# Performance work log

Hardware: AMD Instinct MI355X
Metric: run time of the kernel (lower is better)

The kernel has to match this reference:

```python
import jax, jax.numpy as jnp
import numpy as np

EPS = 1e-5

def layer_norm(x, g, b):
    m = x.mean(-1, keepdims=True)
    v = ((x - m) ** 2).mean(-1, keepdims=True)
    return (x - m) / jnp.sqrt(v + EPS) * g + b

def multihead(qn, kn, vn, Wq, Wk, Wv, causal):
    # Wq/Wk/Wv: [H, E, D]; per-head projections stacked over H (matches per-head Linear loop)
    Q = jnp.einsum('ble,hed->bhld', qn, Wq)
    K = jnp.einsum('bme,hed->bhmd', kn, Wk)
    V = jnp.einsum('bme,hed->bhmd', vn, Wv)
    scale = Q.shape[-1] ** -0.5
    s = jnp.einsum('bhld,bhmd->bhlm', Q, K) * scale
    if causal:
        L, M = s.shape[-2], s.shape[-1]
        mask = jnp.tril(jnp.ones((L, M), dtype=bool))
        s = jnp.where(mask, s, -jnp.inf)
    w = jax.nn.softmax(s, axis=-1)
    o = jnp.einsum('bhlm,bhmd->bhld', w, V)
    return o.mean(axis=1)  # heads are AVERAGED, not concatenated


def setup_inputs() -> dict:
    key = jax.random.key(0)
    ks = jax.random.split(key, 16)
    B, L, E, H, D, FW = 4, 2048, 512, 8, 512, 4
    std = 0.02
    inp = {
        'q': jax.random.normal(ks[0], (B, L, E), jnp.float32),
        'k': jax.random.normal(ks[1], (B, L, E), jnp.float32),
        'v': jax.random.normal(ks[2], (B, L, E), jnp.float32),
        'Wq_s': jax.random.normal(ks[3], (H, E, D), jnp.float32) * std,
        'Wk_s': jax.random.normal(ks[4], (H, E, D), jnp.float32) * std,
        'Wv_s': jax.random.normal(ks[5], (H, E, D), jnp.float32) * std,
        'Wq_c': jax.random.normal(ks[6], (H, E, D), jnp.float32) * std,
        'Wk_c': jax.random.normal(ks[7], (H, E, D), jnp.float32) * std,
        'Wv_c': jax.random.normal(ks[8], (H, E, D), jnp.float32) * std,
        'W1': jax.random.normal(ks[9], (E, FW * E), jnp.float32) * std,
        'b1': jnp.zeros((FW * E,), jnp.float32),
        'W2': jax.random.normal(ks[10], (FW * E, E), jnp.float32) * std,
        'b2': jnp.zeros((E,), jnp.float32),
        'g1': jnp.ones((E,), jnp.float32), 'be1': jnp.zeros((E,), jnp.float32),
        'g2': jnp.ones((E,), jnp.float32), 'be2': jnp.zeros((E,), jnp.float32),
        'g3': jnp.ones((E,), jnp.float32), 'be3': jnp.zeros((E,), jnp.float32),
    }
    return inp


def reference(q, k, v, Wq_s, Wk_s, Wv_s, Wq_c, Wk_c, Wv_c, W1, b1, W2, b2,
              g1, be1, g2, be2, g3, be3):
    # pre-norm causal self-attn (head_size == n_embd, heads averaged)
    q = q + multihead(layer_norm(q, g1, be1), layer_norm(q, g1, be1), layer_norm(q, g1, be1),
                      Wq_s, Wk_s, Wv_s, causal=True)
    # pre-norm cross-attn: only queries are normed; k, v used raw
    q = q + multihead(layer_norm(q, g2, be2), k, v, Wq_c, Wk_c, Wv_c, causal=False)
    # FFN
    h = layer_norm(q, g3, be3)
    h = jax.nn.relu(h @ W1 + b1) @ W2 + b2
    return q + h
```

## Files before the change

kernel.cpp:

```cpp
#include <hip/hip_runtime.h>
#include <cstdint>


typedef __bf16 bf16;
typedef __bf16 bf16x8 __attribute__((ext_vector_type(8)));
typedef float f32x4 __attribute__((ext_vector_type(4)));
typedef int i32x4 __attribute__((ext_vector_type(4)));
typedef int i32x8 __attribute__((ext_vector_type(8)));
typedef unsigned short u16;

static constexpr int Bb = 4, Ls = 2048, Es = 512, Hh = 8, Dd = 512, Ff = 2048;
static constexpr long BL = (long)Bb * Ls;
static constexpr int BIG = 1 << 30;

#define DEV __device__ __forceinline__

DEV u16 f2bf(float x) {
  unsigned u = __float_as_uint(x);
  return (u16)((u + 0x7fffu + ((u >> 16) & 1u)) >> 16);
}

DEV void async16(const void* gp, void* lp) {
  __builtin_amdgcn_global_load_lds(
      (const __attribute__((address_space(1))) void*)gp,
      (__attribute__((address_space(3))) void*)lp, 16, 0, 0);
}

template <int OUT, int SM, int IN8, int O8, bool BIAS, bool RELU, bool CAUSAL, bool RESID>
__global__ __launch_bounds__(256) void gemm128(
    const void* __restrict__ A, const void* __restrict__ Bt, void* __restrict__ Cout,
    const float* __restrict__ bias, const float* __restrict__ resid,
    float* __restrict__ rsum,
    int M, int N, int K, int lda, int ldb, int ldc, int ldct, int tz,
    long sA, long sB, long sC, int dA, int mB, int dC, float alpha) {
  const int m0 = blockIdx.y * 128, n0 = blockIdx.x * 128;
  if (CAUSAL && OUT == 1 && n0 > m0 + 127) return;
  int Keff = K;
  if (CAUSAL && OUT != 1) { int kl = m0 + 128; Keff = kl < K ? kl : K; }

  const int z = blockIdx.z;
  const char* Ab = (const char*)A + (long)(z / dA) * sA;
  const char* Bbp = (const char*)Bt + (long)(z % mB) * sB;
  char* Cb = (char*)Cout + (long)(z / dC) * sC;
  float* RS = (SM != 0) ? (rsum + (long)z * M) : nullptr;

  constexpr int ES = IN8 ? 1 : 2;
  constexpr int KS = IN8 ? 128 : 64;
  const long lasA = (long)lda * ES, lasB = (long)ldb * ES;

  __shared__ char As[16384];
  __shared__ char Bs[16384];

  const int tid = threadIdx.x;
  const int lane = tid & 63;
  const int quad = lane >> 4, r = lane & 15;
  const int wave = tid >> 6;
  const int wm = (wave >> 1) * 64, wn = (wave & 1) * 64;

  f32x4 acc[4][4];
  const f32x4 zero = {0.f, 0.f, 0.f, 0.f};
#pragma unroll
  for (int i = 0; i < 4; ++i)
#pragma unroll
    for (int j = 0; j < 4; ++j) acc[i][j] = zero;

  for (int k0 = 0; k0 < Keff; k0 += KS) {
#pragma unroll
    for (int i = 0; i < 4; ++i) {
      const int c = i * 256 + tid, row = c >> 3;
      const int s = (c & 7) ^ (row & 7);
      async16(Ab + (long)(m0 + row) * lasA + ((long)k0 * ES + s * 16), As + c * 16);
    }
#pragma unroll
    for (int i = 0; i < 4; ++i) {
      const int c = i * 256 + tid, row = c >> 3;
      const int s = (c & 7) ^ (row & 7);
      async16(Bbp + (long)(n0 + row) * lasB + ((long)k0 * ES + s * 16), Bs + c * 16);
    }
    asm volatile("s_waitcnt vmcnt(0)" ::: "memory");
    __syncthreads();

    if (IN8) {
      i32x8 af[4], bw[4];
#pragma unroll
      for (int t = 0; t < 4; ++t) {
        const int Ra = wm + t * 16 + r;
        const char* pa = As + Ra * 128;
        i32x4 alo = *(const i32x4*)(pa + (((2 * quad) ^ (Ra & 7)) * 16));
        i32x4 ahi = *(const i32x4*)(pa + (((2 * quad + 1) ^ (Ra & 7)) * 16));
        af[t] = __builtin_shufflevector(alo, ahi, 0, 1, 2, 3, 4, 5, 6, 7);
        const int Rb = wn + t * 16 + r;
        const char* pb = Bs + Rb * 128;
        i32x4 blo = *(const i32x4*)(pb + (((2 * quad) ^ (Rb & 7)) * 16));
        i32x4 bhi = *(const i32x4*)(pb + (((2 * quad + 1) ^ (Rb & 7)) * 16));
        bw[t] = __builtin_shufflevector(blo, bhi, 0, 1, 2, 3, 4, 5, 6, 7);
      }
#pragma unroll
      for (int i = 0; i < 4; ++i)
#pragma unroll
        for (int j = 0; j < 4; ++j)
          acc[i][j] = __builtin_amdgcn_mfma_scale_f32_16x16x128_f8f6f4(
              af[i], bw[j], acc[i][j], 0, 0, 0, 0x7f7f7f7f, 0, 0x7f7f7f7f);
    } else {
#pragma unroll
      for (int u = 0; u < 2; ++u) {
        bf16x8 af[4], bw[4];
#pragma unroll
        for (int t = 0; t < 4; ++t) {
          const int Ra = wm + t * 16 + r;
          af[t] = *(const bf16x8*)(As + Ra * 128 + (((u * 4 + quad) ^ (Ra & 7)) * 16));
          const int Rb = wn + t * 16 + r;
          bw[t] = *(const bf16x8*)(Bs + Rb * 128 + (((u * 4 + quad) ^ (Rb & 7)) * 16));
        }
#pragma unroll
        for (int i = 0; i < 4; ++i)
#pragma unroll
          for (int j = 0; j < 4; ++j)
            acc[i][j] = __builtin_amdgcn_mfma_f32_16x16x32_bf16(af[i], bw[j], acc[i][j], 0, 0, 0);
      }
    }
    __syncthreads();
  }

#pragma unroll
  for (int i = 0; i < 4; ++i) {
    const int rowb = m0 + wm + i * 16 + quad * 4;
    if (SM == 1) {
      float rpart[4] = {0.f, 0.f, 0.f, 0.f};
#pragma unroll
      for (int j = 0; j < 4; ++j) {
        const int col = n0 + wn + j * 16 + r;
#pragma unroll
        for (int t = 0; t < 4; ++t) {
          float p = __expf(acc[i][j][t] * alpha);
          if (CAUSAL && col > rowb + t) p = 0.f;
          rpart[t] += p;
          if (O8) {
            int w8 = __builtin_amdgcn_cvt_pk_fp8_f32(p, p, 0, false);
            Cb[(long)(rowb + t) * ldc + col] = (char)(w8 & 0xff);
          } else {
            ((u16*)Cb)[(long)(rowb + t) * ldc + col] = f2bf(p);
          }
        }
      }
#pragma unroll
      for (int t = 0; t < 4; ++t) {
        rpart[t] += __shfl_xor(rpart[t], 1);
        rpart[t] += __shfl_xor(rpart[t], 2);
        rpart[t] += __shfl_xor(rpart[t], 4);
        rpart[t] += __shfl_xor(rpart[t], 8);
      }
      if (r == 0) {
#pragma unroll
        for (int t = 0; t < 4; ++t) atomicAdd(RS + rowb + t, rpart[t]);
      }
      continue;
    }
    float rinv[4];
    if (SM == 2) {
#pragma unroll
      for (int t = 0; t < 4; ++t) rinv[t] = alpha / RS[rowb + t];
    }
#pragma unroll
    for (int j = 0; j < 4; ++j) {
      const int col = n0 + wn + j * 16 + r;
      float v[4];
#pragma unroll
      for (int t = 0; t < 4; ++t)
        v[t] = (SM == 2) ? acc[i][j][t] * rinv[t] : acc[i][j][t] * alpha;
      if (BIAS) {
        const float bb = bias[col];
#pragma unroll
        for (int t = 0; t < 4; ++t) v[t] += bb;
      }
      if (RELU) {
#pragma unroll
        for (int t = 0; t < 4; ++t) v[t] = fmaxf(v[t], 0.f);
      }
      if (OUT == 0) {
        float* C = (float*)Cb;
#pragma unroll
        for (int t = 0; t < 4; ++t) {
          long idx = (long)(rowb + t) * ldc + col;
          float o = v[t];
          if (RESID) o += resid[idx];
          C[idx] = o;
        }
      } else {
        if (z >= tz) {
          if (O8) {
            int w8 = __builtin_amdgcn_cvt_pk_fp8_f32(v[0], v[1], 0, false);
            w8 = __builtin_amdgcn_cvt_pk_fp8_f32(v[2], v[3], w8, true);
            *(int*)(Cb + (long)col * ldct + rowb) = w8;
          } else {
            ushort4 p;
            p.x = f2bf(v[0]); p.y = f2bf(v[1]); p.z = f2bf(v[2]); p.w = f2bf(v[3]);
            *(ushort4*)((u16*)Cb + (long)col * ldct + rowb) = p;
          }
        } else {
#pragma unroll
          for (int t = 0; t < 4; ++t) {
            if (O8) {
              int w8 = __builtin_amdgcn_cvt_pk_fp8_f32(v[t], v[t], 0, false);
              Cb[(long)(rowb + t) * ldc + col] = (char)(w8 & 0xff);
            } else {
              ((u16*)Cb)[(long)(rowb + t) * ldc + col] = f2bf(v[t]);
            }
          }
        }
      }
    }
  }
}

template <int F8>
__global__ __launch_bounds__(256) void ln_kernel(
    const float* __restrict__ x, const float* __restrict__ g, const float* __restrict__ be,
    void* __restrict__ y, float* __restrict__ xcopy, int nrows) {
  const int wave = threadIdx.x >> 6, lane = threadIdx.x & 63;
  const long row = (long)blockIdx.x * 4 + wave;
  const float4* xr = (const float4*)(x + row * 512);
  float4 v0 = xr[lane], v1 = xr[lane + 64];
  if (xcopy) {
    float4* c = (float4*)(xcopy + row * 512);
    c[lane] = v0; c[lane + 64] = v1;
  }
  float s = v0.x + v0.y + v0.z + v0.w + v1.x + v1.y + v1.z + v1.w;
#pragma unroll
  for (int o = 32; o >= 1; o >>= 1) s += __shfl_xor(s, o);
  const float m = s * (1.0f / 512.0f);
  float d = (v0.x - m) * (v0.x - m) + (v0.y - m) * (v0.y - m) + (v0.z - m) * (v0.z - m) +
            (v0.w - m) * (v0.w - m) + (v1.x - m) * (v1.x - m) + (v1.y - m) * (v1.y - m) +
            (v1.z - m) * (v1.z - m) + (v1.w - m) * (v1.w - m);
#pragma unroll
  for (int o = 32; o >= 1; o >>= 1) d += __shfl_xor(d, o);
  const float rstd = rsqrtf(d * (1.0f / 512.0f) + 1e-5f);
  const float4* gv = (const float4*)g;
  const float4* bv = (const float4*)be;
  float4 g0 = gv[lane], g1 = gv[lane + 64], b0 = bv[lane], b1 = bv[lane + 64];
  float n0 = (v0.x - m) * rstd * g0.x + b0.x, n1 = (v0.y - m) * rstd * g0.y + b0.y;
  float n2 = (v0.z - m) * rstd * g0.z + b0.z, n3 = (v0.w - m) * rstd * g0.w + b0.w;
  float n4 = (v1.x - m) * rstd * g1.x + b1.x, n5 = (v1.y - m) * rstd * g1.y + b1.y;
  float n6 = (v1.z - m) * rstd * g1.z + b1.z, n7 = (v1.w - m) * rstd * g1.w + b1.w;
  if (F8) {
    char* yr = (char*)y + row * 512;
    int w0 = __builtin_amdgcn_cvt_pk_fp8_f32(n0, n1, 0, false);
    w0 = __builtin_amdgcn_cvt_pk_fp8_f32(n2, n3, w0, true);
    int w1 = __builtin_amdgcn_cvt_pk_fp8_f32(n4, n5, 0, false);
    w1 = __builtin_amdgcn_cvt_pk_fp8_f32(n6, n7, w1, true);
    *(int*)(yr + 4 * lane) = w0;
    *(int*)(yr + 256 + 4 * lane) = w1;
  } else {
    uint2 o0, o1;
    o0.x = (unsigned)f2bf(n0) | ((unsigned)f2bf(n1) << 16);
    o0.y = (unsigned)f2bf(n2) | ((unsigned)f2bf(n3) << 16);
    o1.x = (unsigned)f2bf(n4) | ((unsigned)f2bf(n5) << 16);
    o1.y = (unsigned)f2bf(n6) | ((unsigned)f2bf(n7) << 16);
    uint2* yr = (uint2*)((u16*)y + row * 512);
    yr[lane] = o0; yr[lane + 64] = o1;
  }
}

__global__ __launch_bounds__(256) void cvt_fp8_kernel(const float* __restrict__ x,
                                                      char* __restrict__ y, long n) {
  long i = ((long)blockIdx.x * 256 + threadIdx.x) * 8;
  if (i >= n) return;
  float4 a = *(const float4*)(x + i), b = *(const float4*)(x + i + 4);
  int w0 = __builtin_amdgcn_cvt_pk_fp8_f32(a.x, a.y, 0, false);
  w0 = __builtin_amdgcn_cvt_pk_fp8_f32(a.z, a.w, w0, true);
  int w1 = __builtin_amdgcn_cvt_pk_fp8_f32(b.x, b.y, 0, false);
  w1 = __builtin_amdgcn_cvt_pk_fp8_f32(b.z, b.w, w1, true);
  int2 o; o.x = w0; o.y = w1;
  *(int2*)(y + i) = o;
}

__global__ __launch_bounds__(256) void zero_kernel(float* __restrict__ p) {
  long i = ((long)blockIdx.x * 256 + threadIdx.x) * 4;
  const float4 z4 = {0.f, 0.f, 0.f, 0.f};
  *(float4*)(p + i) = z4;
}

__global__ __launch_bounds__(256) void transpose6(
    const float* __restrict__ s0, const float* __restrict__ s1, const float* __restrict__ s2,
    const float* __restrict__ s3, const float* __restrict__ s4, const float* __restrict__ s5,
    char* __restrict__ out) {
  __shared__ float t[32][33];
  const int set = blockIdx.z >> 3, head = blockIdx.z & 7;
  const float* in = set == 0 ? s0 : set == 1 ? s1 : set == 2 ? s2
                   : set == 3 ? s3 : set == 4 ? s4 : s5;
  const long sW = (long)Es * Dd;
  in += (long)head * sW;
  char* o = out + ((long)set * Hh + head) * sW;
  const int c0 = blockIdx.x * 32, r0 = blockIdx.y * 32;
  const int tx = threadIdx.x & 31, ty = threadIdx.x >> 5;
#pragma unroll
  for (int i = 0; i < 32; i += 8) t[ty + i][tx] = in[(long)(r0 + ty + i) * Dd + (c0 + tx)];
  __syncthreads();
#pragma unroll
  for (int i = 0; i < 32; i += 8) {
    float xv = t[tx][ty + i] * 64.0f;
    o[(long)(c0 + ty + i) * Es + (r0 + tx)] =
        (char)(__builtin_amdgcn_cvt_pk_fp8_f32(xv, xv, 0, false) & 0xff);
  }
}

__global__ __launch_bounds__(256) void transpose_cvt(const float* __restrict__ in,
                                                     u16* __restrict__ out, int R, int C,
                                                     long sIn, long sOut) {
  __shared__ float t[32][33];
  in += (long)blockIdx.z * sIn;
  out += (long)blockIdx.z * sOut;
  const int c0 = blockIdx.x * 32, r0 = blockIdx.y * 32;
  const int tx = threadIdx.x & 31, ty = threadIdx.x >> 5;
#pragma unroll
  for (int i = 0; i < 32; i += 8) t[ty + i][tx] = in[(long)(r0 + ty + i) * C + (c0 + tx)];
  __syncthreads();
#pragma unroll
  for (int i = 0; i < 32; i += 8)
    out[(long)(c0 + ty + i) * R + (r0 + tx)] = f2bf(t[tx][ty + i]);
}

__global__ __launch_bounds__(256) void reduce8_kernel(const float* __restrict__ O,
                                                      float* __restrict__ acc) {
  const long n = (long)Ls * Dd;
  long i = ((long)blockIdx.x * 256 + threadIdx.x) * 4;
  float4 s = *(const float4*)(O + i);
#pragma unroll
  for (int h = 1; h < 8; ++h) {
    float4 t = *(const float4*)(O + (long)h * n + i);
    s.x += t.x; s.y += t.y; s.z += t.z; s.w += t.w;
  }
  float4 a = *(const float4*)(acc + i);
  a.x += s.x; a.y += s.y; a.z += s.z; a.w += s.w;
  *(float4*)(acc + i) = a;
}

__global__ __launch_bounds__(256) void finalize_kernel(const float* __restrict__ slabs,
                                                       const float* __restrict__ resid,
                                                       const float* __restrict__ b2,
                                                       float* __restrict__ out) {
  const long SL = (long)BL * Es;
  long i = ((long)blockIdx.x * 256 + threadIdx.x) * 4;
  float4 a0 = *(const float4*)(slabs + i);
  float4 a1 = *(const float4*)(slabs + SL + i);
  float4 a2 = *(const float4*)(slabs + 2 * SL + i);
  float4 a3 = *(const float4*)(slabs + 3 * SL + i);
  float4 rr = *(const float4*)(resid + i);
  float4 bb = *(const float4*)(b2 + (int)(i & 511));
  float4 o;
  o.x = a0.x + a1.x + a2.x + a3.x + rr.x + bb.x;
  o.y = a0.y + a1.y + a2.y + a3.y + rr.y + bb.y;
  o.z = a0.z + a1.z + a2.z + a3.z + rr.z + bb.z;
  o.w = a0.w + a1.w + a2.w + a3.w + rr.w + bb.w;
  *(float4*)(out + i) = o;
}

extern "C" void kernel_launch(void* const* d_in, const int* in_sizes, int n_in,
                              void* d_out, int out_size, void* d_ws, size_t ws_size,
                              hipStream_t stream) {
  const float* q = (const float*)d_in[0];
  const float* k = (const float*)d_in[1];
  const float* v = (const float*)d_in[2];
  const float* Wq_s = (const float*)d_in[3];
  const float* Wk_s = (const float*)d_in[4];
  const float* Wv_s = (const float*)d_in[5];
  const float* Wq_c = (const float*)d_in[6];
  const float* Wk_c = (const float*)d_in[7];
  const float* Wv_c = (const float*)d_in[8];
  const float* W1 = (const float*)d_in[9];
  const float* b1 = (const float*)d_in[10];
  const float* W2 = (const float*)d_in[11];
  const float* b2 = (const float*)d_in[12];
  const float* g1 = (const float*)d_in[13];
  const float* be1 = (const float*)d_in[14];
  const float* g2 = (const float*)d_in[15];
  const float* be2 = (const float*)d_in[16];
  const float* g3 = (const float*)d_in[17];
  const float* be3 = (const float*)d_in[18];

  char* w = (char*)d_ws;
  size_t off = 0;
  auto alloc = [&](size_t bytes) -> char* {
    char* p = w + off;
    off += (bytes + 255) & ~(size_t)255;
    return p;
  };
  const long sW = (long)Es * Dd;
  const long sQ = (long)Ls * Dd, sS = (long)Ls * Ls;
  const long sBE = (long)Ls * Es;

  u16* Wqst = (u16*)alloc((size_t)Hh * sW * 2);
  u16* Wkst = (u16*)alloc((size_t)Hh * sW * 2);
  u16* Wvst = (u16*)alloc((size_t)Hh * sW * 2);
  u16* Wqct = (u16*)alloc((size_t)Hh * sW * 2);
  u16* Wkct = (u16*)alloc((size_t)Hh * sW * 2);
  u16* Wvct = (u16*)alloc((size_t)Hh * sW * 2);
  u16* W1t = (u16*)alloc((size_t)Es * Ff * 2);
  u16* W2t = (u16*)alloc((size_t)Es * Ff * 2);
  u16* qn = (u16*)alloc((size_t)BL * Es * 2);
  u16* knb = (u16*)alloc((size_t)BL * Es * 2);
  u16* vnb = (u16*)alloc((size_t)BL * Es * 2);
  char* QKV = alloc((size_t)Hh * sQ * 2);
  char* KVx = alloc((size_t)Hh * sQ * 2);
  u16* Vtb = (u16*)alloc((size_t)Hh * sQ * 2);
  char* Sb = alloc((size_t)Hh * sS * 2);
  float* acc1 = (float*)alloc((size_t)BL * Es * 4);
  u16* hbuf = (u16*)alloc((size_t)BL * Ff * 2);
  (void)KVx; (void)Vtb;
  char* Qb8 = QKV;
  char* Kb8 = QKV + (size_t)Hh * sQ;
  float* accF = (float*)Sb;
  float* Osc = (float*)hbuf;
  float* rsum = (float*)W1t;
  char* Wq8 = (char*)Wqst;
  char* qn8 = (char*)qn;
  (void)in_sizes; (void)n_in; (void)out_size; (void)ws_size;

  const dim3 blk(256);
  transpose6<<<dim3(Dd / 32, Es / 32, 48), blk, 0, stream>>>(Wq_s, Wk_s, Wv_s, Wq_c, Wk_c, Wv_c, Wq8);
  cvt_fp8_kernel<<<dim3((unsigned)(BL * Es / 2048)), blk, 0, stream>>>(k, (char*)knb, BL * Es);
  cvt_fp8_kernel<<<dim3((unsigned)(BL * Es / 2048)), blk, 0, stream>>>(v, (char*)vnb, BL * Es);
  zero_kernel<<<dim3(8 * Hh * Ls / 1024), blk, 0, stream>>>(rsum);

  ln_kernel<1><<<dim3((unsigned)(BL / 4)), blk, 0, stream>>>(q, g1, be1, qn8, acc1, (int)BL);

  const float scl = 0.044194173824159216f;
  const float sclS = scl / 4096.0f;
  const float aPV = 0.125f / 64.0f;

  for (int b = 0; b < Bb; ++b) {
    const char* qb8 = qn8 + (long)b * sBE;
    float* rs = rsum + (long)b * Hh * Ls;
    gemm128<1, 0, 1, 1, false, false, false, false><<<dim3(4, 16, 24), blk, 0, stream>>>(
        qb8, Wq8, Qb8, nullptr, nullptr, nullptr, Ls, Dd, Es, Es, Es, Dd, Ls, 16,
        0, sW, sQ, 24, 24, 1, 1.0f);
    gemm128<1, 1, 1, 1, false, false, true, false><<<dim3(16, 16, Hh), blk, 0, stream>>>(
        Qb8, Kb8, Sb, nullptr, nullptr, rs, Ls, Ls, Dd, Dd, Dd, Ls, Ls, BIG,
        sQ, sQ, sS, 1, Hh, 1, sclS);
    gemm128<0, 2, 1, 0, false, false, true, false><<<dim3(4, 16, Hh), blk, 0, stream>>>(
        Sb, Qb8 + 2 * (size_t)Hh * sQ, Osc, nullptr, nullptr, rs, Ls, Dd, Ls, Ls, Ls, Dd, Ls, BIG,
        sS, sQ, sQ * 4, 1, Hh, 1, aPV);
    reduce8_kernel<<<dim3((unsigned)(sQ / 1024)), blk, 0, stream>>>(Osc, acc1 + (long)b * sBE);
  }

  ln_kernel<1><<<dim3((unsigned)(BL / 4)), blk, 0, stream>>>(acc1, g2, be2, qn8, nullptr, (int)BL);

  for (int b = 0; b < Bb; ++b) {
    const char* qb8 = qn8 + (long)b * sBE;
    float* rs = rsum + (long)(4 + b) * Hh * Ls;
    gemm128<1, 0, 1, 1, false, false, false, false><<<dim3(4, 16, 24), blk, 0, stream>>>(
        qb8, Wq8 + 24L * sW, Qb8, nullptr, nullptr, nullptr, Ls, Dd, Es, Es, Es, Dd, Ls, 16,
        (long)BL * Es * 2, sW, sQ, 8, 24, 1, 1.0f);
    gemm128<1, 1, 1, 1, false, false, false, false><<<dim3(16, 16, Hh), blk, 0, stream>>>(
        Qb8, Kb8, Sb, nullptr, nullptr, rs, Ls, Ls, Dd, Dd, Dd, Ls, Ls, BIG,
        sQ, sQ, sS, 1, Hh, 1, sclS);
    gemm128<0, 2, 1, 0, false, false, false, false><<<dim3(4, 16, Hh), blk, 0, stream>>>(
        Sb, Qb8 + 2 * (size_t)Hh * sQ, Osc, nullptr, nullptr, rs, Ls, Dd, Ls, Ls, Ls, Dd, Ls, BIG,
        sS, sQ, sQ * 4, 1, Hh, 1, aPV);
    reduce8_kernel<<<dim3((unsigned)(sQ / 1024)), blk, 0, stream>>>(Osc, acc1 + (long)b * sBE);
  }

  transpose_cvt<<<dim3(Ff / 32, Es / 32, 1), blk, 0, stream>>>(W1, W1t, Es, Ff, 0, 0);
  transpose_cvt<<<dim3(Es / 32, Ff / 32, 1), blk, 0, stream>>>(W2, W2t, Ff, Es, 0, 0);

  ln_kernel<0><<<dim3((unsigned)(BL / 4)), blk, 0, stream>>>(acc1, g3, be3, qn, nullptr, (int)BL);
  gemm128<1, 0, 0, 0, true, true, false, false><<<dim3(Ff / 128, (unsigned)(BL / 128), 1), blk, 0, stream>>>(
      qn, W1t, hbuf, b1, nullptr, nullptr, (int)BL, Ff, Es, Es, Es, Ff, Ff, BIG,
      0, 0, 0, 1, 1, 1, 1.0f);
  gemm128<0, 0, 0, 0, false, false, false, false><<<dim3(Es / 128, (unsigned)(BL / 128), 4), blk, 0, stream>>>(
      hbuf, W2t, accF, nullptr, nullptr, nullptr, (int)BL, Es, 512, Ff, Ff, Es, Es, BIG,
      1024, 1024, (long)BL * Es * 4, 1, 4, 1, 1.0f);
  finalize_kernel<<<dim3((unsigned)(BL * Es / 1024)), blk, 0, stream>>>(accF, acc1, b2, (float*)d_out);
}
```

Before: 1.017 ms.

## Batch attention GEMMs over two batches per launch and store head outputs as bf16

Generalizes the GEMM z-index addressing so that the projection, score and PV GEMMs each process two batch elements per launch instead of one, halving the number of launches and doubling grid size per launch. The per-head PV outputs are now written as bf16 rather than fp32, and a new reduce kernel sums bf16 head slabs for two batches. This targets launch overhead, low occupancy and memory traffic in the reduction, at the cost of more workspace use per launch and reduced precision in the per-head partial outputs.

Measured after the change: 925.8 us. -9.0%, faster.

```diff
diff --git a/kernel.cpp b/kernel.cpp
--- a/kernel.cpp
+++ b/kernel.cpp
@@ -32,17 +32,20 @@
     const float* __restrict__ bias, const float* __restrict__ resid,
     float* __restrict__ rsum,
     int M, int N, int K, int lda, int ldb, int ldc, int ldct, int tz,
-    long sA, long sB, long sC, int dA, int mB, int dC, float alpha) {
+    long sA, int dA, long sAi, int mA, int dAi,
+    long sB, int mB, long sB2, int dB,
+    long sC, int dC, long sCi, int mC, float alpha) {
   const int m0 = blockIdx.y * 128, n0 = blockIdx.x * 128;
-  if (CAUSAL && OUT == 1 && n0 > m0 + 127) return;
+  if (CAUSAL && SM == 1 && n0 > m0 + 127) return;
   int Keff = K;
-  if (CAUSAL && OUT != 1) { int kl = m0 + 128; Keff = kl < K ? kl : K; }
+  if (CAUSAL && SM == 2) { int kl = m0 + 128; Keff = kl < K ? kl : K; }
 
   const int z = blockIdx.z;
-  const char* Ab = (const char*)A + (long)(z / dA) * sA;
-  const char* Bbp = (const char*)Bt + (long)(z % mB) * sB;
-  char* Cb = (char*)Cout + (long)(z / dC) * sC;
+  const char* Ab = (const char*)A + (long)(z / dA) * sA + (long)((z % mA) / dAi) * sAi;
+  const char* Bbp = (const char*)Bt + (long)(z % mB) * sB + (long)(z / dB) * sB2;
+  char* Cb = (char*)Cout + (long)(z / dC) * sC + (long)(z % mC) * sCi;
   float* RS = (SM != 0) ? (rsum + (long)z * M) : nullptr;
+  const int zc = z % mC;
 
   constexpr int ES = IN8 ? 1 : 2;
   constexpr int KS = IN8 ? 128 : 64;
@@ -187,7 +190,7 @@
           C[idx] = o;
         }
       } else {
-        if (z >= tz) {
+        if (zc >= tz) {
           if (O8) {
             int w8 = __builtin_amdgcn_cvt_pk_fp8_f32(v[0], v[1], 0, false);
             w8 = __builtin_amdgcn_cvt_pk_fp8_f32(v[2], v[3], w8, true);
@@ -320,19 +323,25 @@
     out[(long)(c0 + ty + i) * R + (r0 + tx)] = f2bf(t[tx][ty + i]);
 }
 
-__global__ __launch_bounds__(256) void reduce8_kernel(const float* __restrict__ O,
-                                                      float* __restrict__ acc) {
+__global__ __launch_bounds__(256) void reduce8b_kernel(const u16* __restrict__ O,
+                                                       float* __restrict__ acc) {
   const long n = (long)Ls * Dd;
-  long i = ((long)blockIdx.x * 256 + threadIdx.x) * 4;
-  float4 s = *(const float4*)(O + i);
-#pragma unroll
-  for (int h = 1; h < 8; ++h) {
-    float4 t = *(const float4*)(O + (long)h * n + i);
-    s.x += t.x; s.y += t.y; s.z += t.z; s.w += t.w;
-  }
-  float4 a = *(const float4*)(acc + i);
-  a.x += s.x; a.y += s.y; a.z += s.z; a.w += s.w;
-  *(float4*)(acc + i) = a;
+  const u16* Ob = O + (long)blockIdx.y * 8 * n;
+  float* ab = acc + (long)blockIdx.y * (long)Ls * Es;
+  long i = ((long)blockIdx.x * 256 + threadIdx.x) * 8;
+  float s[8] = {0.f, 0.f, 0.f, 0.f, 0.f, 0.f, 0.f, 0.f};
+#pragma unroll
+  for (int h = 0; h < 8; ++h) {
+    bf16x8 t = *(const bf16x8*)(Ob + (long)h * n + i);
+#pragma unroll
+    for (int e = 0; e < 8; ++e) s[e] += (float)t[e];
+  }
+  float4 a0 = *(const float4*)(ab + i);
+  float4 a1 = *(const float4*)(ab + i + 4);
+  a0.x += s[0]; a0.y += s[1]; a0.z += s[2]; a0.w += s[3];
+  a1.x += s[4]; a1.y += s[5]; a1.z += s[6]; a1.w += s[7];
+  *(float4*)(ab + i) = a0;
+  *(float4*)(ab + i + 4) = a1;
 }
 
 __global__ __launch_bounds__(256) void finalize_kernel(const float* __restrict__ slabs,
@@ -386,7 +395,8 @@
     return p;
   };
   const long sW = (long)Es * Dd;
-  const long sQ = (long)Ls * Dd, sS = (long)Ls * Ls;
+  const long sQ = (long)Ls * Dd;
+  const long sS = (long)Ls * Ls;
   const long sBE = (long)Ls * Es;
 
   u16* Wqst = (u16*)alloc((size_t)Hh * sW * 2);
@@ -406,14 +416,13 @@
   char* Sb = alloc((size_t)Hh * sS * 2);
   float* acc1 = (float*)alloc((size_t)BL * Es * 4);
   u16* hbuf = (u16*)alloc((size_t)BL * Ff * 2);
-  (void)KVx; (void)Vtb;
-  char* Qb8 = QKV;
-  char* Kb8 = QKV + (size_t)Hh * sQ;
+  (void)KVx; (void)Vtb; (void)Wkst; (void)Wvst; (void)Wqct; (void)Wkct; (void)Wvct;
+  char* QKVp = QKV;
   float* accF = (float*)Sb;
-  float* Osc = (float*)hbuf;
   float* rsum = (float*)W1t;
   char* Wq8 = (char*)Wqst;
   char* qn8 = (char*)qn;
+  const long tstr = (long)BL * Es * 2;
   (void)in_sizes; (void)n_in; (void)out_size; (void)ws_size;
 
   const dim3 blk(256);
@@ -427,37 +436,56 @@
   const float scl = 0.044194173824159216f;
   const float sclS = scl / 4096.0f;
   const float aPV = 0.125f / 64.0f;
-
-  for (int b = 0; b < Bb; ++b) {
-    const char* qb8 = qn8 + (long)b * sBE;
-    float* rs = rsum + (long)b * Hh * Ls;
-    gemm128<1, 0, 1, 1, false, false, false, false><<<dim3(4, 16, 24), blk, 0, stream>>>(
-        qb8, Wq8, Qb8, nullptr, nullptr, nullptr, Ls, Dd, Es, Es, Es, Dd, Ls, 16,
-        0, sW, sQ, 24, 24, 1, 1.0f);
-    gemm128<1, 1, 1, 1, false, false, true, false><<<dim3(16, 16, Hh), blk, 0, stream>>>(
-        Qb8, Kb8, Sb, nullptr, nullptr, rs, Ls, Ls, Dd, Dd, Dd, Ls, Ls, BIG,
-        sQ, sQ, sS, 1, Hh, 1, sclS);
-    gemm128<0, 2, 1, 0, false, false, true, false><<<dim3(4, 16, Hh), blk, 0, stream>>>(
-        Sb, Qb8 + 2 * (size_t)Hh * sQ, Osc, nullptr, nullptr, rs, Ls, Dd, Ls, Ls, Ls, Dd, Ls, BIG,
-        sS, sQ, sQ * 4, 1, Hh, 1, aPV);
-    reduce8_kernel<<<dim3((unsigned)(sQ / 1024)), blk, 0, stream>>>(Osc, acc1 + (long)b * sBE);
+  const float* np = nullptr;
+
+  for (int p = 0; p < 2; ++p) {
+    const char* qp8 = qn8 + (long)p * 2 * sBE;
+    float* rsS = rsum + (long)p * 16 * Ls;
+    gemm128<1, 0, 1, 1, false, false, false, false><<<dim3(4, 16, 48), blk, 0, stream>>>(
+        qp8, Wq8, QKVp, np, np, nullptr, Ls, Dd, Es, Es, Es, Dd, Ls, 16,
+        sBE, 24, 0, 24, 8,
+        sW, 24, 0, 1,
+        24 * sQ, 24, sQ, 24,
+        1.0f);
+    gemm128<1, 1, 1, 1, false, false, true, false><<<dim3(16, 16, 16), blk, 0, stream>>>(
+        QKVp, QKVp + 8 * sQ, Sb, np, np, rsS, Ls, Ls, Dd, Dd, Dd, Ls, Ls, BIG,
+        24 * sQ, 8, sQ, 8, 1,
+        sQ, 8, 24 * sQ, 8,
+        8 * sS, 8, sS, 8,
+        sclS);
+    gemm128<1, 2, 1, 0, false, false, true, false><<<dim3(4, 16, 16), blk, 0, stream>>>(
+        Sb, QKVp + 16 * sQ, hbuf, np, np, rsS, Ls, Dd, Ls, Ls, Ls, Dd, Ls, BIG,
+        8 * sS, 8, sS, 8, 1,
+        sQ, 8, 24 * sQ, 8,
+        8 * sQ * 2, 8, sQ * 2, 8,
+        aPV);
+    reduce8b_kernel<<<dim3(512, 2), blk, 0, stream>>>(hbuf, acc1 + (long)p * 2 * sBE);
   }
 
   ln_kernel<1><<<dim3((unsigned)(BL / 4)), blk, 0, stream>>>(acc1, g2, be2, qn8, nullptr, (int)BL);
 
-  for (int b = 0; b < Bb; ++b) {
-    const char* qb8 = qn8 + (long)b * sBE;
-    float* rs = rsum + (long)(4 + b) * Hh * Ls;
-    gemm128<1, 0, 1, 1, false, false, false, false><<<dim3(4, 16, 24), blk, 0, stream>>>(
-        qb8, Wq8 + 24L * sW, Qb8, nullptr, nullptr, nullptr, Ls, Dd, Es, Es, Es, Dd, Ls, 16,
-        (long)BL * Es * 2, sW, sQ, 8, 24, 1, 1.0f);
-    gemm128<1, 1, 1, 1, false, false, false, false><<<dim3(16, 16, Hh), blk, 0, stream>>>(
-        Qb8, Kb8, Sb, nullptr, nullptr, rs, Ls, Ls, Dd, Dd, Dd, Ls, Ls, BIG,
-        sQ, sQ, sS, 1, Hh, 1, sclS);
-    gemm128<0, 2, 1, 0, false, false, false, false><<<dim3(4, 16, Hh), blk, 0, stream>>>(
-        Sb, Qb8 + 2 * (size_t)Hh * sQ, Osc, nullptr, nullptr, rs, Ls, Dd, Ls, Ls, Ls, Dd, Ls, BIG,
-        sS, sQ, sQ * 4, 1, Hh, 1, aPV);
-    reduce8_kernel<<<dim3((unsigned)(sQ / 1024)), blk, 0, stream>>>(Osc, acc1 + (long)b * sBE);
+  for (int p = 0; p < 2; ++p) {
+    const char* qp8 = qn8 + (long)p * 2 * sBE;
+    float* rsS = rsum + (long)(32 + p * 16) * Ls;
+    gemm128<1, 0, 1, 1, false, false, false, false><<<dim3(4, 16, 48), blk, 0, stream>>>(
+        qp8, Wq8 + 24 * sW, QKVp, np, np, nullptr, Ls, Dd, Es, Es, Es, Dd, Ls, 16,
+        sBE, 24, tstr, 24, 8,
+        sW, 24, 0, 1,
+        24 * sQ, 24, sQ, 24,
+        1.0f);
+    gemm128<1, 1, 1, 1, false, false, false, false><<<dim3(16, 16, 16), blk, 0, stream>>>(
+        QKVp, QKVp + 8 * sQ, Sb, np, np, rsS, Ls, Ls, Dd, Dd, Dd, Ls, Ls, BIG,
+        24 * sQ, 8, sQ, 8, 1,
+        sQ, 8, 24 * sQ, 8,
+        8 * sS, 8, sS, 8,
+        sclS);
+    gemm128<1, 2, 1, 0, false, false, false, false><<<dim3(4, 16, 16), blk, 0, stream>>>(
+        Sb, QKVp + 16 * sQ, hbuf, np, np, rsS, Ls, Dd, Ls, Ls, Ls, Dd, Ls, BIG,
+        8 * sS, 8, sS, 8, 1,
+        sQ, 8, 24 * sQ, 8,
+        8 * sQ * 2, 8, sQ * 2, 8,
+        aPV);
+    reduce8b_kernel<<<dim3(512, 2), blk, 0, stream>>>(hbuf, acc1 + (long)p * 2 * sBE);
   }
 
   transpose_cvt<<<dim3(Ff / 32, Es / 32, 1), blk, 0, stream>>>(W1, W1t, Es, Ff, 0, 0);
@@ -465,10 +493,15 @@
 
   ln_kernel<0><<<dim3((unsigned)(BL / 4)), blk, 0, stream>>>(acc1, g3, be3, qn, nullptr, (int)BL);
   gemm128<1, 0, 0, 0, true, true, false, false><<<dim3(Ff / 128, (unsigned)(BL / 128), 1), blk, 0, stream>>>(
-      qn, W1t, hbuf, b1, nullptr, nullptr, (int)BL, Ff, Es, Es, Es, Ff, Ff, BIG,
-      0, 0, 0, 1, 1, 1, 1.0f);
+      qn, W1t, hbuf, b1, np, nullptr, (int)BL, Ff, Es, Es, Es, Ff, Ff, BIG,
+      0, 1, 0, 1, 1,
+      0, 1, 0, 1,
+      0, 1, 0, 1, 1.0f);
   gemm128<0, 0, 0, 0, false, false, false, false><<<dim3(Es / 128, (unsigned)(BL / 128), 4), blk, 0, stream>>>(
-      hbuf, W2t, accF, nullptr, nullptr, nullptr, (int)BL, Es, 512, Ff, Ff, Es, Es, BIG,
-      1024, 1024, (long)BL * Es * 4, 1, 4, 1, 1.0f);
+      hbuf, W2t, accF, np, np, nullptr, (int)BL, Es, 512, Ff, Ff, Es, Es, BIG,
+      1024, 1, 0, 1, 1,
+      0, 1, 1024, 1,
+      (long)BL * Es * 4, 1, 0, 1,
+      1.0f);
   finalize_kernel<<<dim3((unsigned)(BL * Es / 1024)), blk, 0, stream>>>(accF, acc1, b2, (float*)d_out);
 }
```
